# Performance work log

Hardware: AMD Instinct MI355X
Metric: run time of the kernel (lower is better)

The kernel has to match this reference:

```python
import jax, jax.numpy as jnp
import numpy as np

EPS = 1e-8
B, T, D = 2, 512, 64
L = 4        # n_layers
NPASS = 2    # n_recursive_passes


def setup_inputs() -> dict:
    key = jax.random.key(0)
    ks = jax.random.split(key, 8)
    H = D // 2
    r = lambda k, shape, s=0.05: jax.random.normal(k, shape, dtype=jnp.float32) * s
    return {
        "basin_seq": jax.random.normal(ks[0], (B, T, D), dtype=jnp.float32),
        "basin_coords": r(ks[1], (D,), 0.1),
        "W_temp": r(ks[2], (L, 1, D)),
        "b_temp": jnp.zeros((L, 1), jnp.float32),
        "res_scale": jnp.full((L,), 0.1, jnp.float32),
        "W_fb": r(ks[3], (L, D, 2 * D)),
        "b_fb": jnp.zeros((L, D), jnp.float32),
        "Wc1": r(ks[4], (H, D)),
        "bc1": jnp.zeros((H,), jnp.float32),
        "Wc2": r(ks[5], (D, H)),
        "bc2": jnp.zeros((D,), jnp.float32),
        "Wu": r(ks[6], (D, 2 * D)),
        "bu": jnp.zeros((D,), jnp.float32),
        "res_scale_g": jnp.asarray(1.0, jnp.float32),
    }


def _project_to_simplex(x):
    s = jax.nn.softplus(x)
    s = s / (s.sum(axis=-1, keepdims=True) + EPS)
    return jnp.maximum(s, EPS)


def _qfi_attention_weights(x, temperature):
    # x: (B,T,D); temperature: scalar
    p = _project_to_simplex(x)
    # fisher_rao_distance_simplex renormalizes its inputs again
    p = p / (p.sum(axis=-1, keepdims=True) + EPS)
    # pairwise Bhattacharyya-like inner product: (B,T,T,D) broadcast -> (B,T,T)
    inner = jnp.sqrt(p[:, :, None, :] * p[:, None, :, :] + EPS).sum(axis=-1)
    inner = jnp.clip(inner, -1.0 + 1e-6, 1.0 - 1e-6)
    d = 2.0 * jnp.arccos(inner)                      # Fisher-Rao distance (B,T,T)
    logits = -d / jnp.maximum(temperature, 1e-6)
    return jax.nn.softmax(logits, axis=-1)


def _forward(basin_seq, basin_coords, W_temp, b_temp, res_scale, W_fb, b_fb,
             Wc1, bc1, Wc2, bc2, Wu, bu, res_scale_g):
    x = basin_seq
    current_basin = basin_coords                     # (D,)
    layer_states = [[None] * L for _ in range(NPASS)]
    for p_idx in range(NPASS):
        for l in range(L):
            prev = layer_states[p_idx - 1][l] if p_idx > 0 else None
            if prev is not None:
                combined = jnp.concatenate([x, prev], axis=-1)          # (B,T,2D)
                gate = jax.nn.sigmoid(combined @ W_fb[l].T + b_fb[l])   # (B,T,D)
                x = x * gate + prev * (1.0 - gate)
            # BasinCoupledQFIAttention (dropout inactive in eval)
            tm = jax.nn.sigmoid(W_temp[l] @ current_basin + b_temp[l]) + 0.5
            temperature = jax.lax.stop_gradient(tm.mean())  # torch uses .item()
            w = _qfi_attention_weights(x, temperature)
            x_attn = jnp.einsum('bij,bjd->bid', w, x)
            x = x + res_scale[l] * (x_attn - x)
            layer_states[p_idx][l] = x
        # holographic encode: mean-pool then compress MLP (tanh, tanh)
        pooled = x.mean(axis=1)                                         # (B,D)
        hidden_basin = jnp.tanh(jnp.tanh(pooled @ Wc1.T + bc1) @ Wc2.T + bc2)
        if p_idx < NPASS - 1:
            aggregated = hidden_basin.mean(axis=0)                      # (D,)
            comb = jnp.concatenate([current_basin, aggregated], axis=-1)
            g = jax.nn.sigmoid(Wu @ comb + bu)
            current_basin = current_basin * (1.0 - g) + aggregated * g
    output = x + 0.01 * res_scale_g * (x - basin_seq)
    return output


def reference(basin_seq, basin_coords, W_temp, b_temp, res_scale, W_fb, b_fb,
              Wc1, bc1, Wc2, bc2, Wu, bu, res_scale_g):
    return _forward(basin_seq, basin_coords, W_temp, b_temp, res_scale, W_fb,
                    b_fb, Wc1, bc1, Wc2, bc2, Wu, bu, res_scale_g)
```

## Files before the change

### kernel.cpp

```cpp
#include <hip/hip_runtime.h>
#include <math.h>

#define EPSF 1e-8f
#define Tn 512
#define Dn 64
#define ROWS 1024
#define NELEM 65536

typedef _Float16 half_t;
typedef __attribute__((ext_vector_type(4))) _Float16 half4;

__device__ __forceinline__ float sigmoidf_(float x){ return 1.0f/(1.0f+expf(-x)); }
__device__ __forceinline__ float softplusf_(float x){ return fmaxf(x,0.0f) + log1pf(expf(-fabsf(x))); }

__device__ __forceinline__ float wrs(float v){
  #pragma unroll
  for (int off=1; off<64; off<<=1) v += __shfl_xor(v, off, 64);
  return v;
}
__device__ __forceinline__ float wrm(float v){
  #pragma unroll
  for (int off=1; off<64; off<<=1) v = fmaxf(v, __shfl_xor(v, off, 64));
  return v;
}

__device__ __forceinline__ void pnorm_w(float xg, int b, int r, int row, int d,
                                        float* __restrict__ sbuf_out,
                                        half_t* __restrict__ sTh_out){
  float s = softplusf_(xg);
  float sum = wrs(s);
  float p = fmaxf(s/(sum+EPSF), EPSF);
  float s2 = wrs(p);
  float sq = sqrtf(p/(s2+EPSF));
  sbuf_out[(size_t)row*Dn + d] = sq;
  sTh_out[(size_t)b*Dn*Tn + (size_t)d*Tn + r] = (half_t)sq;
}

__global__ __launch_bounds__(256) void k_prologue(
    const float* __restrict__ basin_seq, float* __restrict__ sA, half_t* __restrict__ sThA,
    half_t* __restrict__ xhBS,
    const float* __restrict__ W_temp, const float* __restrict__ b_temp,
    const float* __restrict__ cb0, float* __restrict__ temps){
  int tid = threadIdx.x, wid = tid>>6, lane = tid&63;
  if (blockIdx.x < 256){
    int row = blockIdx.x*4 + wid;
    float xv = basin_seq[(size_t)row*Dn+lane];
    xhBS[(size_t)row*Dn+lane] = (half_t)xv;
    pnorm_w(xv, row>>9, row&511, row, lane, sA, sThA);
  } else if (tid < 64){
    float cbv = cb0[tid];
    #pragma unroll
    for (int l=0;l<4;l++){
      float v = wrs(W_temp[l*Dn + tid]*cbv);
      if (tid==0) temps[l] = sigmoidf_(v + b_temp[l]) + 0.5f;
    }
  }
}

__device__ __forceinline__ void gate_dot2(float (*comb)[128], float* gred,
                                          const float* __restrict__ Wfb, int tid, int lane){
  int dd = tid >> 3, k8 = tid & 7;
  const float4* wp = (const float4*)(Wfb + (size_t)dd*128 + k8*16);
  float4 w0 = wp[0], w1 = wp[1], w2 = wp[2], w3 = wp[3];
  float ga[2];
  #pragma unroll
  for (int i=0;i<2;i++){
    float4 c0 = *(const float4*)&comb[i][k8*16];
    float4 c1 = *(const float4*)&comb[i][k8*16+4];
    float4 c2 = *(const float4*)&comb[i][k8*16+8];
    float4 c3 = *(const float4*)&comb[i][k8*16+12];
    ga[i] = w0.x*c0.x + w0.y*c0.y + w0.z*c0.z + w0.w*c0.w
          + w1.x*c1.x + w1.y*c1.y + w1.z*c1.z + w1.w*c1.w
          + w2.x*c2.x + w2.y*c2.y + w2.z*c2.z + w2.w*c2.w
          + w3.x*c3.x + w3.y*c3.y + w3.z*c3.z + w3.w*c3.w;
  }
  #pragma unroll
  for (int off=1; off<8; off<<=1){
    ga[0] += __shfl_xor(ga[0],off,64); ga[1] += __shfl_xor(ga[1],off,64);
  }
  if ((lane&7)==0){ gred[dd*3+0]=ga[0]; gred[dd*3+1]=ga[1]; }
}

template<int MODE>
__global__ __launch_bounds__(512) void k_attn(
    const float* __restrict__ xin, const half_t* __restrict__ xh,
    const float* __restrict__ sbuf, const half_t* __restrict__ sTh,
    const float* __restrict__ temps, const float* __restrict__ res_scale, int l,
    float* __restrict__ xout, half_t* __restrict__ xh_out,
    float* __restrict__ sbuf_out, half_t* __restrict__ sTh_out,
    const float* __restrict__ Wfb, const float* __restrict__ bfb,
    const float* __restrict__ prev,
    const float* __restrict__ basin_seq, const float* __restrict__ rsg){
  __shared__ __align__(16) union {
    float part[8*512];
    float pvp[32*2*64];
  } u;
  __shared__ __align__(8) float P[512*2];
  __shared__ __align__(8) float s_i[64*2];
  __shared__ float redw[2][8][2];
  __shared__ __align__(16) float comb[2][128];
  __shared__ float gred[64*3];

  int tid = threadIdx.x, wav = tid>>6, lane = tid&63;
  int row0 = blockIdx.x*2, b = row0>>9, r0 = row0&511;
  int i_ = tid>>6, d_ = lane;

  float xi_pre = 0.f, prev_pre = 0.f;
  if (tid < 128){
    s_i[d_*2 + i_] = sbuf[(size_t)(row0+i_)*Dn + d_];
    xi_pre = xin[(size_t)(row0+i_)*Dn + d_];
    if constexpr (MODE == 2) prev_pre = prev[(size_t)(row0+i_)*Dn + d_];
  }
  __syncthreads();

  float invT = 1.0f/fmaxf(temps[l], 1e-6f);
  {
    int g = tid & 127, kq = tid >> 7;
    const half4* sT4 = (const half4*)(sTh + (size_t)b*Dn*Tn);
    float4 a0 = {0,0,0,0}, a1 = a0;
    int kb = kq*16;
    #pragma unroll
    for (int kk=0; kk<16; ++kk){
      int k = kb + kk;
      half4 vh = sT4[(size_t)k*128 + g];
      float vx=(float)vh.x, vy=(float)vh.y, vz=(float)vh.z, vw=(float)vh.w;
      float2 si = *(const float2*)&s_i[k*2];
      a0.x=fmaf(si.x,vx,a0.x); a0.y=fmaf(si.x,vy,a0.y);
      a0.z=fmaf(si.x,vz,a0.z); a0.w=fmaf(si.x,vw,a0.w);
      a1.x=fmaf(si.y,vx,a1.x); a1.y=fmaf(si.y,vy,a1.y);
      a1.z=fmaf(si.y,vz,a1.z); a1.w=fmaf(si.y,vw,a1.w);
    }
    *(float4*)&u.part[(0*4+kq)*512 + g*4] = a0;
    *(float4*)&u.part[(1*4+kq)*512 + g*4] = a1;
  }
  __syncthreads();
  {
    int j = tid;
    float a0 = u.part[0*512+j] + u.part[1*512+j] + u.part[2*512+j] + u.part[3*512+j];
    float a1 = u.part[4*512+j] + u.part[5*512+j] + u.part[6*512+j] + u.part[7*512+j];
    float l0 = -2.0f*acosf(fminf(fmaxf(a0,-1.0f+1e-6f),1.0f-1e-6f))*invT;
    float l1 = -2.0f*acosf(fminf(fmaxf(a1,-1.0f+1e-6f),1.0f-1e-6f))*invT;
    float m0=wrm(l0), m1=wrm(l1);
    if (lane==0){ redw[0][wav][0]=m0; redw[0][wav][1]=m1; }
    __syncthreads();
    float mv0=redw[0][0][0], mv1=redw[0][0][1];
    #pragma unroll
    for (int w=1;w<8;w++){ mv0=fmaxf(mv0,redw[0][w][0]); mv1=fmaxf(mv1,redw[0][w][1]); }
    float e0=expf(l0-mv0), e1=expf(l1-mv1);
    float2 ev = {e0,e1};
    *(float2*)&P[j*2] = ev;
    float q0=wrs(e0), q1=wrs(e1);
    if (lane==0){ redw[1][wav][0]=q0; redw[1][wav][1]=q1; }
  }
  __syncthreads();
  {
    int jg = tid>>4, dq = tid&15;
    const half4* x4 = (const half4*)(xh + (size_t)b*Tn*Dn);
    float4 o0={0,0,0,0}, o1=o0;
    int jb = jg*16;
    #pragma unroll
    for (int jj=0; jj<16; ++jj){
      int j = jb + jj;
      half4 xvh = x4[(size_t)j*16 + dq];
      float xx=(float)xvh.x, xy=(float)xvh.y, xz=(float)xvh.z, xw=(float)xvh.w;
      float2 pw = *(const float2*)&P[j*2];
      o0.x=fmaf(pw.x,xx,o0.x); o0.y=fmaf(pw.x,xy,o0.y);
      o0.z=fmaf(pw.x,xz,o0.z); o0.w=fmaf(pw.x,xw,o0.w);
      o1.x=fmaf(pw.y,xx,o1.x); o1.y=fmaf(pw.y,xy,o1.y);
      o1.z=fmaf(pw.y,xz,o1.z); o1.w=fmaf(pw.y,xw,o1.w);
    }
    *(float4*)&u.pvp[(jg*2+0)*64 + dq*4] = o0;
    *(float4*)&u.pvp[(jg*2+1)*64 + dq*4] = o1;
  }
  __syncthreads();
  float o = 0.f;
  if (tid < 128){
    float ss = 0.f;
    #pragma unroll
    for (int jg=0; jg<32; ++jg) ss += u.pvp[(jg*2+i_)*64+d_];
    float sv = 0.f;
    #pragma unroll
    for (int w=0;w<8;w++) sv += redw[1][w][i_];
    float attn = ss/sv;
    o = xi_pre + res_scale[l]*(attn - xi_pre);
  }
  if constexpr (MODE == 0){
    if (tid < 128){
      xout[(size_t)(row0+i_)*Dn + d_] = o;
      xh_out[(size_t)(row0+i_)*Dn + d_] = (half_t)o;
      pnorm_w(o, b, r0+i_, row0+i_, d_, sbuf_out, sTh_out);
    }
  } else if constexpr (MODE == 1){
    if (tid < 128) xout[(size_t)(row0+i_)*Dn + d_] = o;
  } else if constexpr (MODE == 2){
    if (tid < 128){
      comb[i_][d_] = o;
      comb[i_][64+d_] = prev_pre;
    }
    __syncthreads();
    gate_dot2(comb, gred, Wfb, tid, lane);
    __syncthreads();
    if (tid < 128){
      float g = sigmoidf_(gred[d_*3+i_] + bfb[d_]);
      float xg = o*g + prev_pre*(1.0f-g);
      xout[(size_t)(row0+i_)*Dn + d_] = xg;
      xh_out[(size_t)(row0+i_)*Dn + d_] = (half_t)xg;
      pnorm_w(xg, b, r0+i_, row0+i_, d_, sbuf_out, sTh_out);
    }
  } else {
    if (tid < 128){
      float c = 0.01f * rsg[0];
      xout[(size_t)(row0+i_)*Dn + d_] = o + c*(o - basin_seq[(size_t)(row0+i_)*Dn + d_]);
    }
  }
}

__global__ __launch_bounds__(256) void k_basinprep(
    const float* __restrict__ st3, const float* __restrict__ st0,
    const float* __restrict__ W_fb, const float* __restrict__ b_fb,
    float* __restrict__ xA, half_t* __restrict__ xhA,
    float* __restrict__ sA, half_t* __restrict__ sThA,
    const float* __restrict__ Wc1, const float* __restrict__ bc1,
    const float* __restrict__ Wc2, const float* __restrict__ bc2,
    const float* __restrict__ Wu,  const float* __restrict__ bu,
    const float* __restrict__ cb_in, float* __restrict__ cb_out,
    const float* __restrict__ W_temp, const float* __restrict__ b_temp,
    float* __restrict__ temps){
  int tid = threadIdx.x, wid = tid>>6, lane = tid&63;
  __shared__ __align__(16) float comb4[4][128];
  __shared__ float pooled[128];
  __shared__ float h1[64];
  __shared__ float hb[128];
  __shared__ float combb[128];
  if (blockIdx.x < 256){
    int row = blockIdx.x*4 + wid;
    float xv = st3[(size_t)row*Dn+lane];
    float pvv = st0[(size_t)row*Dn+lane];
    comb4[wid][lane] = xv; comb4[wid][64+lane] = pvv;
    __syncthreads();
    const float4* W  = (const float4*)(W_fb + (size_t)lane*128);
    const float4* c4 = (const float4*)comb4[wid];
    float g0=0.f,g1=0.f;
    #pragma unroll
    for (int k=0;k<32;k+=2){
      float4 w0=W[k],   c0=c4[k];
      float4 w1=W[k+1], c1=c4[k+1];
      g0 += w0.x*c0.x + w0.y*c0.y + w0.z*c0.z + w0.w*c0.w;
      g1 += w1.x*c1.x + w1.y*c1.y + w1.z*c1.z + w1.w*c1.w;
    }
    float g = sigmoidf_(g0+g1 + b_fb[lane]);
    float xg = xv*g + pvv*(1.0f-g);
    xA[(size_t)row*Dn+lane] = xg;
    xhA[(size_t)row*Dn+lane] = (half_t)xg;
    pnorm_w(xg, row>>9, row&511, row, lane, sA, sThA);
  } else {
    if (tid < 128){
      int b = tid >> 6, d = tid & 63;
      float acc=0.f;
      const float* xb = st3 + (size_t)b*Tn*Dn + d;
      for (int t=0;t<Tn;t++) acc += xb[(size_t)t*Dn];
      pooled[tid] = acc * (1.0f/Tn);
    }
    __syncthreads();
    if (tid < 64){
      int b = tid >> 5, h = tid & 31;
      float acc=0.f;
      #pragma unroll 8
      for (int d2=0; d2<64; d2++) acc += pooled[b*64+d2]*Wc1[h*64+d2];
      h1[tid] = tanhf(acc + bc1[h]);
    }
    __syncthreads();
    if (tid < 128){
      int b = tid >> 6, d = tid & 63;
      float acc=0.f;
      #pragma unroll 8
      for (int h2=0; h2<32; h2++) acc += h1[b*32+h2]*Wc2[d*32+h2];
      hb[tid] = tanhf(acc + bc2[d]);
    }
    __syncthreads();
    if (tid < 64){
      float agg = 0.5f*(hb[tid] + hb[64+tid]);
      combb[tid] = cb_in[tid];
      combb[64+tid] = agg;
    }
    __syncthreads();
    if (tid < 64){
      float acc=0.f;
      #pragma unroll 8
      for (int k=0;k<128;k++) acc += Wu[tid*128+k]*combb[k];
      float g = sigmoidf_(acc + bu[tid]);
      float nb = combb[tid]*(1.0f-g) + combb[64+tid]*g;
      cb_out[tid] = nb;
      #pragma unroll
      for (int l=0;l<4;l++){
        float v = wrs(W_temp[l*Dn + tid]*nb);
        if (tid==0) temps[l] = sigmoidf_(v + b_temp[l]) + 0.5f;
      }
    }
  }
}

extern "C" void kernel_launch(void* const* d_in, const int* in_sizes, int n_in,
                              void* d_out, int out_size, void* d_ws, size_t ws_size,
                              hipStream_t stream) {
  const float* basin_seq    = (const float*)d_in[0];
  const float* basin_coords = (const float*)d_in[1];
  const float* W_temp       = (const float*)d_in[2];
  const float* b_temp       = (const float*)d_in[3];
  const float* res_scale    = (const float*)d_in[4];
  const float* W_fb         = (const float*)d_in[5];
  const float* b_fb         = (const float*)d_in[6];
  const float* Wc1          = (const float*)d_in[7];
  const float* bc1          = (const float*)d_in[8];
  const float* Wc2          = (const float*)d_in[9];
  const float* bc2          = (const float*)d_in[10];
  const float* Wu           = (const float*)d_in[11];
  const float* bu           = (const float*)d_in[12];
  const float* rsg          = (const float*)d_in[13];
  float* out = (float*)d_out;
  float* ws  = (float*)d_ws;

  const size_t N = NELEM;
  float* sA    = ws;
  float* sB    = ws + N;
  float* st    = ws + 2*N;
  float* xA    = ws + 6*N;
  float* xB    = ws + 7*N;
  half_t* sThA = (half_t*)(ws + 8*N);
  half_t* sThB = (half_t*)(ws + 8*N + N/2);
  half_t* xhBS = (half_t*)(ws + 9*N);
  half_t* xhA  = (half_t*)(ws + 9*N + N/2);
  half_t* xhB  = (half_t*)(ws + 10*N);
  float* temps = ws + 10*N + N/2;
  float* cb    = ws + 10*N + N/2 + 64;
  float* st0 = st, *st1 = st+N, *st2 = st+2*N, *st3 = st+3*N;

  const int GA = 512;

  k_prologue<<<257,256,0,stream>>>(basin_seq, sA, sThA, xhBS, W_temp, b_temp, basin_coords, temps);
  k_attn<0><<<GA,512,0,stream>>>(basin_seq, xhBS, sA, sThA, temps, res_scale, 0,
                                 st0, xhA, sB, sThB, nullptr,nullptr,nullptr,nullptr,nullptr);
  k_attn<0><<<GA,512,0,stream>>>(st0, xhA, sB, sThB, temps, res_scale, 1,
                                 st1, xhB, sA, sThA, nullptr,nullptr,nullptr,nullptr,nullptr);
  k_attn<0><<<GA,512,0,stream>>>(st1, xhB, sA, sThA, temps, res_scale, 2,
                                 st2, xhA, sB, sThB, nullptr,nullptr,nullptr,nullptr,nullptr);
  k_attn<1><<<GA,512,0,stream>>>(st2, xhA, sB, sThB, temps, res_scale, 3,
                                 st3, nullptr, nullptr, nullptr, nullptr,nullptr,nullptr,nullptr,nullptr);
  k_basinprep<<<257,256,0,stream>>>(st3, st0, W_fb, b_fb, xA, xhA, sA, sThA,
                                    Wc1, bc1, Wc2, bc2, Wu, bu,
                                    basin_coords, cb, W_temp, b_temp, temps);
  k_attn<2><<<GA,512,0,stream>>>(xA, xhA, sA, sThA, temps, res_scale, 0,
                                 xB, xhB, sB, sThB,
                                 W_fb + (size_t)1*Dn*2*Dn, b_fb + 1*Dn, st1, nullptr,nullptr);
  k_attn<2><<<GA,512,0,stream>>>(xB, xhB, sB, sThB, temps, res_scale, 1,
                                 xA, xhA, sA, sThA,
                                 W_fb + (size_t)2*Dn*2*Dn, b_fb + 2*Dn, st2, nullptr,nullptr);
  k_attn<2><<<GA,512,0,stream>>>(xA, xhA, sA, sThA, temps, res_scale, 2,
                                 xB, xhB, sB, sThB,
                                 W_fb + (size_t)3*Dn*2*Dn, b_fb + 3*Dn, st3, nullptr,nullptr);
  k_attn<3><<<GA,512,0,stream>>>(xB, xhB, sB, sThB, temps, res_scale, 3,
                                 out, nullptr, nullptr, nullptr,
                                 nullptr,nullptr,nullptr, basin_seq, rsg);
}
```

Baseline: 175.0 us.

## Drop fp16 transposed copies; compute similarity row-wise from fp32 buffers

Removes the half-precision transposed sqrt-probability buffer and the half copy of x. The similarity stage now has each thread read one full fp32 row of sqrt-probabilities and dot it against the two query rows, and the PV stage reads fp32 x directly. This drops the partial-sum reduction and its barrier, uses fast __expf, and splits the mean-pool in basinprep across more threads. In exchange each thread strides through 256-byte rows, giving uncoalesced global loads, and memory traffic for the operands doubles.

```diff
diff --git a/kernel.cpp b/kernel.cpp
--- a/kernel.cpp
+++ b/kernel.cpp
@@ -4,14 +4,10 @@
 #define EPSF 1e-8f
 #define Tn 512
 #define Dn 64
-#define ROWS 1024
 #define NELEM 65536
 
-typedef _Float16 half_t;
-typedef __attribute__((ext_vector_type(4))) _Float16 half4;
-
-__device__ __forceinline__ float sigmoidf_(float x){ return 1.0f/(1.0f+expf(-x)); }
-__device__ __forceinline__ float softplusf_(float x){ return fmaxf(x,0.0f) + log1pf(expf(-fabsf(x))); }
+__device__ __forceinline__ float sigmoidf_(float x){ return 1.0f/(1.0f+__expf(-x)); }
+__device__ __forceinline__ float softplusf_(float x){ return fmaxf(x,0.0f) + log1pf(__expf(-fabsf(x))); }
 
 __device__ __forceinline__ float wrs(float v){
   #pragma unroll
@@ -24,29 +20,22 @@
   return v;
 }
 
-__device__ __forceinline__ void pnorm_w(float xg, int b, int r, int row, int d,
-                                        float* __restrict__ sbuf_out,
-                                        half_t* __restrict__ sTh_out){
+__device__ __forceinline__ void pnorm_w(float xg, int row, int d, float* __restrict__ sr_out){
   float s = softplusf_(xg);
   float sum = wrs(s);
   float p = fmaxf(s/(sum+EPSF), EPSF);
   float s2 = wrs(p);
-  float sq = sqrtf(p/(s2+EPSF));
-  sbuf_out[(size_t)row*Dn + d] = sq;
-  sTh_out[(size_t)b*Dn*Tn + (size_t)d*Tn + r] = (half_t)sq;
+  sr_out[(size_t)row*Dn + d] = sqrtf(p/(s2+EPSF));
 }
 
 __global__ __launch_bounds__(256) void k_prologue(
-    const float* __restrict__ basin_seq, float* __restrict__ sA, half_t* __restrict__ sThA,
-    half_t* __restrict__ xhBS,
+    const float* __restrict__ basin_seq, float* __restrict__ sA,
     const float* __restrict__ W_temp, const float* __restrict__ b_temp,
     const float* __restrict__ cb0, float* __restrict__ temps){
   int tid = threadIdx.x, wid = tid>>6, lane = tid&63;
   if (blockIdx.x < 256){
     int row = blockIdx.x*4 + wid;
-    float xv = basin_seq[(size_t)row*Dn+lane];
-    xhBS[(size_t)row*Dn+lane] = (half_t)xv;
-    pnorm_w(xv, row>>9, row&511, row, lane, sA, sThA);
+    pnorm_w(basin_seq[(size_t)row*Dn+lane], row, lane, sA);
   } else if (tid < 64){
     float cbv = cb0[tid];
     #pragma unroll
@@ -83,101 +72,89 @@
 
 template<int MODE>
 __global__ __launch_bounds__(512) void k_attn(
-    const float* __restrict__ xin, const half_t* __restrict__ xh,
-    const float* __restrict__ sbuf, const half_t* __restrict__ sTh,
+    const float* __restrict__ xin, const float* __restrict__ sr,
     const float* __restrict__ temps, const float* __restrict__ res_scale, int l,
-    float* __restrict__ xout, half_t* __restrict__ xh_out,
-    float* __restrict__ sbuf_out, half_t* __restrict__ sTh_out,
+    float* __restrict__ xout, float* __restrict__ sr_out,
     const float* __restrict__ Wfb, const float* __restrict__ bfb,
     const float* __restrict__ prev,
     const float* __restrict__ basin_seq, const float* __restrict__ rsg){
-  __shared__ __align__(16) union {
-    float part[8*512];
-    float pvp[32*2*64];
-  } u;
-  __shared__ __align__(8) float P[512*2];
-  __shared__ __align__(8) float s_i[64*2];
+  __shared__ __align__(16) float pvp[64*64];
+  __shared__ __align__(8)  float P[512*2];
+  __shared__ __align__(16) float s01[64*2];
   __shared__ float redw[2][8][2];
   __shared__ __align__(16) float comb[2][128];
   __shared__ float gred[64*3];
 
   int tid = threadIdx.x, wav = tid>>6, lane = tid&63;
-  int row0 = blockIdx.x*2, b = row0>>9, r0 = row0&511;
+  int row0 = blockIdx.x*2, b = row0>>9;
   int i_ = tid>>6, d_ = lane;
 
   float xi_pre = 0.f, prev_pre = 0.f;
   if (tid < 128){
-    s_i[d_*2 + i_] = sbuf[(size_t)(row0+i_)*Dn + d_];
+    s01[d_*2 + i_] = sr[(size_t)(row0+i_)*Dn + d_];
     xi_pre = xin[(size_t)(row0+i_)*Dn + d_];
     if constexpr (MODE == 2) prev_pre = prev[(size_t)(row0+i_)*Dn + d_];
   }
   __syncthreads();
 
   float invT = 1.0f/fmaxf(temps[l], 1e-6f);
+
+  float a0=0.f, a1=0.f, b0=0.f, b1=0.f;
   {
-    int g = tid & 127, kq = tid >> 7;
-    const half4* sT4 = (const half4*)(sTh + (size_t)b*Dn*Tn);
-    float4 a0 = {0,0,0,0}, a1 = a0;
-    int kb = kq*16;
-    #pragma unroll
-    for (int kk=0; kk<16; ++kk){
-      int k = kb + kk;
-      half4 vh = sT4[(size_t)k*128 + g];
-      float vx=(float)vh.x, vy=(float)vh.y, vz=(float)vh.z, vw=(float)vh.w;
-      float2 si = *(const float2*)&s_i[k*2];
-      a0.x=fmaf(si.x,vx,a0.x); a0.y=fmaf(si.x,vy,a0.y);
-      a0.z=fmaf(si.x,vz,a0.z); a0.w=fmaf(si.x,vw,a0.w);
-      a1.x=fmaf(si.y,vx,a1.x); a1.y=fmaf(si.y,vy,a1.y);
-      a1.z=fmaf(si.y,vz,a1.z); a1.w=fmaf(si.y,vw,a1.w);
-    }
-    *(float4*)&u.part[(0*4+kq)*512 + g*4] = a0;
-    *(float4*)&u.part[(1*4+kq)*512 + g*4] = a1;
-  }
-  __syncthreads();
+    const float4* rj4 = (const float4*)(sr + (size_t)b*Tn*Dn + (size_t)tid*Dn);
+    const float4* sp  = (const float4*)s01;
+    #pragma unroll 8
+    for (int c=0;c<16;++c){
+      float4 x4 = rj4[c];
+      float4 sa = sp[2*c], sb = sp[2*c+1];
+      a0 = fmaf(x4.x, sa.x, a0); a1 = fmaf(x4.x, sa.y, a1);
+      b0 = fmaf(x4.y, sa.z, b0); b1 = fmaf(x4.y, sa.w, b1);
+      a0 = fmaf(x4.z, sb.x, a0); a1 = fmaf(x4.z, sb.y, a1);
+      b0 = fmaf(x4.w, sb.z, b0); b1 = fmaf(x4.w, sb.w, b1);
+    }
+    a0 += b0; a1 += b1;
+  }
   {
-    int j = tid;
-    float a0 = u.part[0*512+j] + u.part[1*512+j] + u.part[2*512+j] + u.part[3*512+j];
-    float a1 = u.part[4*512+j] + u.part[5*512+j] + u.part[6*512+j] + u.part[7*512+j];
-    float l0 = -2.0f*acosf(fminf(fmaxf(a0,-1.0f+1e-6f),1.0f-1e-6f))*invT;
-    float l1 = -2.0f*acosf(fminf(fmaxf(a1,-1.0f+1e-6f),1.0f-1e-6f))*invT;
+    float c0 = fminf(fmaxf(a0,-1.0f+1e-6f),1.0f-1e-6f);
+    float c1 = fminf(fmaxf(a1,-1.0f+1e-6f),1.0f-1e-6f);
+    float l0 = -2.0f*acosf(c0)*invT;
+    float l1 = -2.0f*acosf(c1)*invT;
     float m0=wrm(l0), m1=wrm(l1);
     if (lane==0){ redw[0][wav][0]=m0; redw[0][wav][1]=m1; }
     __syncthreads();
     float mv0=redw[0][0][0], mv1=redw[0][0][1];
     #pragma unroll
     for (int w=1;w<8;w++){ mv0=fmaxf(mv0,redw[0][w][0]); mv1=fmaxf(mv1,redw[0][w][1]); }
-    float e0=expf(l0-mv0), e1=expf(l1-mv1);
-    float2 ev = {e0,e1};
-    *(float2*)&P[j*2] = ev;
+    float e0=__expf(l0-mv0), e1=__expf(l1-mv1);
+    *(float2*)&P[tid*2] = make_float2(e0,e1);
     float q0=wrs(e0), q1=wrs(e1);
     if (lane==0){ redw[1][wav][0]=q0; redw[1][wav][1]=q1; }
   }
   __syncthreads();
   {
     int jg = tid>>4, dq = tid&15;
-    const half4* x4 = (const half4*)(xh + (size_t)b*Tn*Dn);
-    float4 o0={0,0,0,0}, o1=o0;
+    const float4* x4p = (const float4*)(xin + (size_t)b*Tn*Dn);
+    float4 o0={0,0,0,0}, o1={0,0,0,0};
     int jb = jg*16;
-    #pragma unroll
+    #pragma unroll 8
     for (int jj=0; jj<16; ++jj){
       int j = jb + jj;
-      half4 xvh = x4[(size_t)j*16 + dq];
-      float xx=(float)xvh.x, xy=(float)xvh.y, xz=(float)xvh.z, xw=(float)xvh.w;
+      float4 xv = x4p[(size_t)j*16 + dq];
       float2 pw = *(const float2*)&P[j*2];
-      o0.x=fmaf(pw.x,xx,o0.x); o0.y=fmaf(pw.x,xy,o0.y);
-      o0.z=fmaf(pw.x,xz,o0.z); o0.w=fmaf(pw.x,xw,o0.w);
-      o1.x=fmaf(pw.y,xx,o1.x); o1.y=fmaf(pw.y,xy,o1.y);
-      o1.z=fmaf(pw.y,xz,o1.z); o1.w=fmaf(pw.y,xw,o1.w);
-    }
-    *(float4*)&u.pvp[(jg*2+0)*64 + dq*4] = o0;
-    *(float4*)&u.pvp[(jg*2+1)*64 + dq*4] = o1;
+      o0.x=fmaf(pw.x,xv.x,o0.x); o0.y=fmaf(pw.x,xv.y,o0.y);
+      o0.z=fmaf(pw.x,xv.z,o0.z); o0.w=fmaf(pw.x,xv.w,o0.w);
+      o1.x=fmaf(pw.y,xv.x,o1.x); o1.y=fmaf(pw.y,xv.y,o1.y);
+      o1.z=fmaf(pw.y,xv.z,o1.z); o1.w=fmaf(pw.y,xv.w,o1.w);
+    }
+    *(float4*)&pvp[(jg*2+0)*64 + dq*4] = o0;
+    *(float4*)&pvp[(jg*2+1)*64 + dq*4] = o1;
   }
   __syncthreads();
   float o = 0.f;
   if (tid < 128){
     float ss = 0.f;
     #pragma unroll
-    for (int jg=0; jg<32; ++jg) ss += u.pvp[(jg*2+i_)*64+d_];
+    for (int jg=0; jg<32; ++jg) ss += pvp[(jg*2+i_)*64+d_];
     float sv = 0.f;
     #pragma unroll
     for (int w=0;w<8;w++) sv += redw[1][w][i_];
@@ -187,8 +164,7 @@
   if constexpr (MODE == 0){
     if (tid < 128){
       xout[(size_t)(row0+i_)*Dn + d_] = o;
-      xh_out[(size_t)(row0+i_)*Dn + d_] = (half_t)o;
-      pnorm_w(o, b, r0+i_, row0+i_, d_, sbuf_out, sTh_out);
+      pnorm_w(o, row0+i_, d_, sr_out);
     }
   } else if constexpr (MODE == 1){
     if (tid < 128) xout[(size_t)(row0+i_)*Dn + d_] = o;
@@ -204,8 +180,7 @@
       float g = sigmoidf_(gred[d_*3+i_] + bfb[d_]);
       float xg = o*g + prev_pre*(1.0f-g);
       xout[(size_t)(row0+i_)*Dn + d_] = xg;
-      xh_out[(size_t)(row0+i_)*Dn + d_] = (half_t)xg;
-      pnorm_w(xg, b, r0+i_, row0+i_, d_, sbuf_out, sTh_out);
+      pnorm_w(xg, row0+i_, d_, sr_out);
     }
   } else {
     if (tid < 128){
@@ -218,8 +193,7 @@
 __global__ __launch_bounds__(256) void k_basinprep(
     const float* __restrict__ st3, const float* __restrict__ st0,
     const float* __restrict__ W_fb, const float* __restrict__ b_fb,
-    float* __restrict__ xA, half_t* __restrict__ xhA,
-    float* __restrict__ sA, half_t* __restrict__ sThA,
+    float* __restrict__ xA, float* __restrict__ sA,
     const float* __restrict__ Wc1, const float* __restrict__ bc1,
     const float* __restrict__ Wc2, const float* __restrict__ bc2,
     const float* __restrict__ Wu,  const float* __restrict__ bu,
@@ -228,6 +202,7 @@
     float* __restrict__ temps){
   int tid = threadIdx.x, wid = tid>>6, lane = tid&63;
   __shared__ __align__(16) float comb4[4][128];
+  __shared__ float partial[256];
   __shared__ float pooled[128];
   __shared__ float h1[64];
   __shared__ float hb[128];
@@ -251,30 +226,40 @@
     float g = sigmoidf_(g0+g1 + b_fb[lane]);
     float xg = xv*g + pvv*(1.0f-g);
     xA[(size_t)row*Dn+lane] = xg;
-    xhA[(size_t)row*Dn+lane] = (half_t)xg;
-    pnorm_w(xg, row>>9, row&511, row, lane, sA, sThA);
+    pnorm_w(xg, row, lane, sA);
   } else {
-    if (tid < 128){
-      int b = tid >> 6, d = tid & 63;
-      float acc=0.f;
-      const float* xb = st3 + (size_t)b*Tn*Dn + d;
-      for (int t=0;t<Tn;t++) acc += xb[(size_t)t*Dn];
-      pooled[tid] = acc * (1.0f/Tn);
+    {
+      int bb = tid>>7, rem = tid&127, d = rem>>1, h = rem&1;
+      const float* xb = st3 + (size_t)bb*Tn*Dn + d;
+      float acc0=0.f,acc1=0.f,acc2=0.f,acc3=0.f;
+      int t0 = h*256;
+      for (int t=0;t<256;t+=4){
+        acc0 += xb[(size_t)(t0+t  )*Dn];
+        acc1 += xb[(size_t)(t0+t+1)*Dn];
+        acc2 += xb[(size_t)(t0+t+2)*Dn];
+        acc3 += xb[(size_t)(t0+t+3)*Dn];
+      }
+      partial[tid] = acc0+acc1+acc2+acc3;
+    }
+    __syncthreads();
+    if (tid < 128){
+      int bb = tid>>6, d = tid&63;
+      pooled[tid] = (partial[bb*128+d*2] + partial[bb*128+d*2+1]) * (1.0f/Tn);
     }
     __syncthreads();
     if (tid < 64){
-      int b = tid >> 5, h = tid & 31;
+      int bb = tid >> 5, h = tid & 31;
       float acc=0.f;
       #pragma unroll 8
-      for (int d2=0; d2<64; d2++) acc += pooled[b*64+d2]*Wc1[h*64+d2];
+      for (int d2=0; d2<64; d2++) acc += pooled[bb*64+d2]*Wc1[h*64+d2];
       h1[tid] = tanhf(acc + bc1[h]);
     }
     __syncthreads();
     if (tid < 128){
-      int b = tid >> 6, d = tid & 63;
+      int bb = tid >> 6, d = tid & 63;
       float acc=0.f;
       #pragma unroll 8
-      for (int h2=0; h2<32; h2++) acc += h1[b*32+h2]*Wc2[d*32+h2];
+      for (int h2=0; h2<32; h2++) acc += h1[bb*32+h2]*Wc2[d*32+h2];
       hb[tid] = tanhf(acc + bc2[d]);
     }
     __syncthreads();
@@ -321,44 +306,40 @@
   float* ws  = (float*)d_ws;
 
   const size_t N = NELEM;
-  float* sA    = ws;
-  float* sB    = ws + N;
-  float* st    = ws + 2*N;
+  float* srA   = ws;
+  float* srB   = ws + N;
+  float* st0   = ws + 2*N;
+  float* st1   = ws + 3*N;
+  float* st2   = ws + 4*N;
+  float* st3   = ws + 5*N;
   float* xA    = ws + 6*N;
   float* xB    = ws + 7*N;
-  half_t* sThA = (half_t*)(ws + 8*N);
-  half_t* sThB = (half_t*)(ws + 8*N + N/2);
-  half_t* xhBS = (half_t*)(ws + 9*N);
-  half_t* xhA  = (half_t*)(ws + 9*N + N/2);
-  half_t* xhB  = (half_t*)(ws + 10*N);
-  float* temps = ws + 10*N + N/2;
-  float* cb    = ws + 10*N + N/2 + 64;
-  float* st0 = st, *st1 = st+N, *st2 = st+2*N, *st3 = st+3*N;
+  float* temps = ws + 8*N;
+  float* cb    = ws + 8*N + 64;
 
   const int GA = 512;
 
-  k_prologue<<<257,256,0,stream>>>(basin_seq, sA, sThA, xhBS, W_temp, b_temp, basin_coords, temps);
-  k_attn<0><<<GA,512,0,stream>>>(basin_seq, xhBS, sA, sThA, temps, res_scale, 0,
-                                 st0, xhA, sB, sThB, nullptr,nullptr,nullptr,nullptr,nullptr);
-  k_attn<0><<<GA,512,0,stream>>>(st0, xhA, sB, sThB, temps, res_scale, 1,
-                                 st1, xhB, sA, sThA, nullptr,nullptr,nullptr,nullptr,nullptr);
-  k_attn<0><<<GA,512,0,stream>>>(st1, xhB, sA, sThA, temps, res_scale, 2,
-                                 st2, xhA, sB, sThB, nullptr,nullptr,nullptr,nullptr,nullptr);
-  k_attn<1><<<GA,512,0,stream>>>(st2, xhA, sB, sThB, temps, res_scale, 3,
-                                 st3, nullptr, nullptr, nullptr, nullptr,nullptr,nullptr,nullptr,nullptr);
-  k_basinprep<<<257,256,0,stream>>>(st3, st0, W_fb, b_fb, xA, xhA, sA, sThA,
+  k_prologue<<<257,256,0,stream>>>(basin_seq, srA, W_temp, b_temp, basin_coords, temps);
+  k_attn<0><<<GA,512,0,stream>>>(basin_seq, srA, temps, res_scale, 0,
+                                 st0, srB, nullptr,nullptr,nullptr,nullptr,nullptr);
+  k_attn<0><<<GA,512,0,stream>>>(st0, srB, temps, res_scale, 1,
+                                 st1, srA, nullptr,nullptr,nullptr,nullptr,nullptr);
+  k_attn<0><<<GA,512,0,stream>>>(st1, srA, temps, res_scale, 2,
+                                 st2, srB, nullptr,nullptr,nullptr,nullptr,nullptr);
+  k_attn<1><<<GA,512,0,stream>>>(st2, srB, temps, res_scale, 3,
+                                 st3, nullptr, nullptr,nullptr,nullptr,nullptr,nullptr);
+  k_basinprep<<<257,256,0,stream>>>(st3, st0, W_fb, b_fb, xA, srA,
                                     Wc1, bc1, Wc2, bc2, Wu, bu,
                                     basin_coords, cb, W_temp, b_temp, temps);
-  k_attn<2><<<GA,512,0,stream>>>(xA, xhA, sA, sThA, temps, res_scale, 0,
-                                 xB, xhB, sB, sThB,
+  k_attn<2><<<GA,512,0,stream>>>(xA, srA, temps, res_scale, 0,
+                                 xB, srB,
                                  W_fb + (size_t)1*Dn*2*Dn, b_fb + 1*Dn, st1, nullptr,nullptr);
-  k_attn<2><<<GA,512,0,stream>>>(xB, xhB, sB, sThB, temps, res_scale, 1,
-                                 xA, xhA, sA, sThA,
+  k_attn<2><<<GA,512,0,stream>>>(xB, srB, temps, res_scale, 1,
+                                 xA, srA,
                                  W_fb + (size_t)2*Dn*2*Dn, b_fb + 2*Dn, st2, nullptr,nullptr);
-  k_attn<2><<<GA,512,0,stream>>>(xA, xhA, sA, sThA, temps, res_scale, 2,
-                                 xB, xhB, sB, sThB,
+  k_attn<2><<<GA,512,0,stream>>>(xA, srA, temps, res_scale, 2,
+                                 xB, srB,
                                  W_fb + (size_t)3*Dn*2*Dn, b_fb + 3*Dn, st3, nullptr,nullptr);
-  k_attn<3><<<GA,512,0,stream>>>(xB, xhB, sB, sThB, temps, res_scale, 3,
-                                 out, nullptr, nullptr, nullptr,
-                                 nullptr,nullptr,nullptr, basin_seq, rsg);
-}
+  k_attn<3><<<GA,512,0,stream>>>(xB, srB, temps, res_scale, 3,
+                                 out, nullptr, nullptr,nullptr,nullptr, basin_seq, rsg);
+}
```

Result: slower. 235.2 us (+34.4%).
